# Performance work log

Measured on AMD Instinct MI355X. Metric: run time of the kernel, lower is better.

## Reference

```python
import jax, jax.numpy as jnp
import numpy as np

N_NODES = 20000      # rows of mask
MAX_DEG = 64         # padded slots per node (softmax dim)
DEG = 16             # actual edges per node
E = N_NODES * DEG    # 320000 edges
D_X = 64
D_REF = 64
IN_SIZE = D_X + D_REF   # 128
OUT_SIZE = 64
NEG_FILL = -9e15


def setup_inputs() -> dict:
    key = jax.random.key(0)
    k1, k2, k3, k4 = jax.random.split(key, 4)
    x = jax.random.normal(k1, (E, D_X), dtype=jnp.float32)
    ref = jax.random.normal(k2, (E, D_REF), dtype=jnp.float32)
    mask = jnp.ones((N_NODES, MAX_DEG), dtype=bool)  # only its shape is used
    # valid (node, slot) pairs: each node owns slots 0..DEG-1
    rows = jnp.repeat(jnp.arange(N_NODES, dtype=jnp.int32), DEG)
    cols = jnp.tile(jnp.arange(DEG, dtype=jnp.int32), N_NODES)
    x_idx = jnp.stack([rows, cols], axis=0)  # [2, E]
    # Linear(in_size, out_size) params (torch convention: W [out, in])
    bound = 1.0 / np.sqrt(IN_SIZE)
    W = jax.random.uniform(k3, (OUT_SIZE, IN_SIZE), jnp.float32, -bound, bound)
    b = jax.random.uniform(k4, (OUT_SIZE,), jnp.float32, -bound, bound)
    return {"x": x, "ref": ref, "mask": mask, "x_idx": x_idx, "W": W, "b": b}


def reference(x, ref, mask, x_idx, W, b):
    # w = tanh(Linear(cat([x, ref], -1)))  -> [E, OUT]
    w = jnp.tanh(jnp.concatenate([x, ref], axis=-1) @ W.T + b)
    # scatter into dense [N, MAX_DEG, OUT] padded with a huge negative value
    dense = jnp.full(mask.shape + (w.shape[-1],), NEG_FILL, dtype=w.dtype)
    dense = dense.at[x_idx[0], x_idx[1]].set(w)
    # softmax over the slot dimension (dim=-2), then gather back to edges
    dense = jax.nn.softmax(dense, axis=-2)
    return dense[x_idx[0], x_idx[1]]
```

## Files before the change

kernel.cpp:

```cpp
#include <hip/hip_runtime.h>


#define DEG 16
#define DCH 64
#define KDIM 128
#define NPW 10

typedef __bf16 bf16x8 __attribute__((ext_vector_type(8)));
typedef float f32x4 __attribute__((ext_vector_type(4)));

__device__ __forceinline__ bf16x8 cvt8(f32x4 a, f32x4 b) {
    bf16x8 r;
    r[0] = (__bf16)a[0]; r[1] = (__bf16)a[1]; r[2] = (__bf16)a[2]; r[3] = (__bf16)a[3];
    r[4] = (__bf16)b[0]; r[5] = (__bf16)b[1]; r[6] = (__bf16)b[2]; r[7] = (__bf16)b[3];
    return r;
}

__device__ __forceinline__ void load_node(const float* __restrict__ xr,
                                          const float* __restrict__ rr,
                                          f32x4* __restrict__ raw) {
    raw[0] = *(const f32x4*)(xr);
    raw[1] = *(const f32x4*)(xr + 4);
    raw[2] = *(const f32x4*)(xr + 32);
    raw[3] = *(const f32x4*)(xr + 36);
    raw[4] = *(const f32x4*)(rr);
    raw[5] = *(const f32x4*)(rr + 4);
    raw[6] = *(const f32x4*)(rr + 32);
    raw[7] = *(const f32x4*)(rr + 36);
}

__global__ __launch_bounds__(256, 2) void attn_fused(
    const float* __restrict__ x, const float* __restrict__ ref,
    const float* __restrict__ W, const float* __restrict__ bias,
    float* __restrict__ out)
{
    const int lane = threadIdx.x & 63;
    const int wid  = blockIdx.x * 4 + (threadIdx.x >> 6);
    const int r16  = lane & 15;
    const int g    = lane >> 4;

    bf16x8 Bf[4][4];
#pragma unroll
    for (int u = 0; u < 4; ++u) {
        const float* wr = W + (u * 16 + r16) * KDIM;
#pragma unroll
        for (int t = 0; t < 4; ++t) {
            const float* p = wr + t * 32 + g * 8;
            Bf[t][u] = cvt8(*(const f32x4*)p, *(const f32x4*)(p + 4));
        }
    }
    float bv[4];
#pragma unroll
    for (int u = 0; u < 4; ++u) bv[u] = bias[u * 16 + r16];

    const size_t e0 = (size_t)wid * (NPW * DEG);

    f32x4 bufA[8], bufB[8];
    load_node(x + (e0 + r16) * DCH + g * 8, ref + (e0 + r16) * DCH + g * 8, bufA);

#pragma unroll
    for (int ni = 0; ni < NPW; ++ni) {
        f32x4* cur = (ni & 1) ? bufB : bufA;
        f32x4* nxt = (ni & 1) ? bufA : bufB;
        if (ni + 1 < NPW) {
            const size_t e = e0 + (size_t)(ni + 1) * DEG;
            load_node(x + (e + r16) * DCH + g * 8, ref + (e + r16) * DCH + g * 8, nxt);
        }

        f32x4 acc[4];
#pragma unroll
        for (int u = 0; u < 4; ++u)
            acc[u] = (f32x4){bv[u], bv[u], bv[u], bv[u]};
#pragma unroll
        for (int t = 0; t < 4; ++t) {
            bf16x8 Af = cvt8(cur[2 * t], cur[2 * t + 1]);
#pragma unroll
            for (int u = 0; u < 4; ++u)
                acc[u] = __builtin_amdgcn_mfma_f32_16x16x32_bf16(Af, Bf[t][u], acc[u], 0, 0, 0);
        }

        float* ob = out + (e0 + (size_t)ni * DEG) * DCH;
#pragma unroll
        for (int u = 0; u < 4; ++u) {
            float p[4];
            float s = 0.f;
#pragma unroll
            for (int r = 0; r < 4; ++r) {
                float z = acc[u][r];
                float e = __expf(2.f * z);
                float w = 1.f - 2.f * __builtin_amdgcn_rcpf(e + 1.f);
                p[r] = __expf(w);
                s += p[r];
            }
            s += __shfl_xor(s, 16);
            s += __shfl_xor(s, 32);
            float inv = __builtin_amdgcn_rcpf(s);
#pragma unroll
            for (int r = 0; r < 4; ++r)
                ob[(g * 4 + r) * DCH + u * 16 + r16] = p[r] * inv;
        }
    }
}

extern "C" void kernel_launch(void* const* d_in, const int* in_sizes, int n_in,
                              void* d_out, int out_size, void* d_ws, size_t ws_size,
                              hipStream_t stream) {
    const float* x   = (const float*)d_in[0];
    const float* ref = (const float*)d_in[1];
    const float* W   = (const float*)d_in[4];
    const float* b   = (const float*)d_in[5];
    float* out = (float*)d_out;

    attn_fused<<<500, 256, 0, stream>>>(x, ref, W, b, out);
}
```

Measured before the change: 223.0 us.

## Stage node inputs via async global-to-LDS loads with swizzled double buffering

Replaces per-lane register prefetch of x/ref rows with global_load_lds direct-to-LDS copies into two per-wave XOR-swizzled slots. Waits are driven by explicit vmcnt counters, and each node's tile is read back from LDS before issuing the copy for node k+2. The goal is fully coalesced 16-byte loads and deeper prefetch without using registers. The cost is 64KB of LDS per block, which may limit occupancy, plus fragile hand-tuned waitcnt values and an extra LDS round trip.

```diff
diff --git a/kernel.cpp b/kernel.cpp
--- a/kernel.cpp
+++ b/kernel.cpp
@@ -1,10 +1,11 @@
 #include <hip/hip_runtime.h>
+#include <stdint.h>
 
 
 #define DEG 16
 #define DCH 64
 #define KDIM 128
-#define NPW 10
+#define ITERS 10
 
 typedef __bf16 bf16x8 __attribute__((ext_vector_type(8)));
 typedef float f32x4 __attribute__((ext_vector_type(4)));
@@ -16,17 +17,25 @@
     return r;
 }
 
-__device__ __forceinline__ void load_node(const float* __restrict__ xr,
-                                          const float* __restrict__ rr,
-                                          f32x4* __restrict__ raw) {
-    raw[0] = *(const f32x4*)(xr);
-    raw[1] = *(const f32x4*)(xr + 4);
-    raw[2] = *(const f32x4*)(xr + 32);
-    raw[3] = *(const f32x4*)(xr + 36);
-    raw[4] = *(const f32x4*)(rr);
-    raw[5] = *(const f32x4*)(rr + 4);
-    raw[6] = *(const f32x4*)(rr + 32);
-    raw[7] = *(const f32x4*)(rr + 36);
+__device__ __forceinline__ void gload16(const float* gsrc, void* ldst) {
+    __builtin_amdgcn_global_load_lds(
+        (const __attribute__((address_space(1))) uint32_t*)gsrc,
+        (__attribute__((address_space(3))) uint32_t*)ldst, 16, 0, 0);
+}
+
+__device__ __forceinline__ void stage_node(const float* __restrict__ x,
+                                           const float* __restrict__ ref,
+                                           int node, char* slot, int lane) {
+    const int rq = lane >> 4;
+    const int cb = (lane & 15) * 16;
+#pragma unroll
+    for (int i = 0; i < 8; ++i) {
+        const int r  = (i & 3) * 4 + rq;
+        const int sc = cb ^ ((r & 7) << 5);
+        const float* base = (i < 4) ? x : ref;
+        const float* src  = base + (size_t)(node * DEG + r) * DCH + (sc >> 2);
+        gload16(src, slot + i * 1024);
+    }
 }
 
 __global__ __launch_bounds__(256, 2) void attn_fused(
@@ -34,10 +43,14 @@
     const float* __restrict__ W, const float* __restrict__ bias,
     float* __restrict__ out)
 {
+    __shared__ __align__(16) char smem[65536];
+
     const int lane = threadIdx.x & 63;
-    const int wid  = blockIdx.x * 4 + (threadIdx.x >> 6);
+    const int wv   = threadIdx.x >> 6;
+    const int wid  = blockIdx.x * 4 + wv;
     const int r16  = lane & 15;
     const int g    = lane >> 4;
+    const int sw16 = (r16 & 7) << 5;
 
     bf16x8 Bf[4][4];
 #pragma unroll
@@ -53,33 +66,47 @@
 #pragma unroll
     for (int u = 0; u < 4; ++u) bv[u] = bias[u * 16 + r16];
 
-    const size_t e0 = (size_t)wid * (NPW * DEG);
+    char* slot0 = smem + wv * 16384;
+    char* slot1 = slot0 + 8192;
+    const int base = wid * ITERS;
 
-    f32x4 bufA[8], bufB[8];
-    load_node(x + (e0 + r16) * DCH + g * 8, ref + (e0 + r16) * DCH + g * 8, bufA);
+    stage_node(x, ref, base + 0, slot0, lane);
+    stage_node(x, ref, base + 1, slot1, lane);
+    __builtin_amdgcn_sched_barrier(0);
 
+#pragma unroll 1
+    for (int k = 0; k < ITERS; ++k) {
+        if (k == 0) { asm volatile("s_waitcnt vmcnt(8)" ::: "memory"); }
+        else        { asm volatile("s_waitcnt vmcnt(24)" ::: "memory"); }
+        __builtin_amdgcn_sched_barrier(0);
+
+        char* S = (k & 1) ? slot1 : slot0;
+
+        bf16x8 Af[4];
 #pragma unroll
-    for (int ni = 0; ni < NPW; ++ni) {
-        f32x4* cur = (ni & 1) ? bufB : bufA;
-        f32x4* nxt = (ni & 1) ? bufA : bufB;
-        if (ni + 1 < NPW) {
-            const size_t e = e0 + (size_t)(ni + 1) * DEG;
-            load_node(x + (e + r16) * DCH + g * 8, ref + (e + r16) * DCH + g * 8, nxt);
+        for (int t = 0; t < 4; ++t) {
+            const int colb = (t & 1) * 128 + g * 32;
+            const char* p = S + (t >> 1) * 4096 + r16 * 256 + (colb ^ sw16);
+            f32x4 a0 = *(const f32x4*)p;
+            f32x4 a1 = *(const f32x4*)(p + 16);
+            Af[t] = cvt8(a0, a1);
         }
+        asm volatile("s_waitcnt lgkmcnt(0)" ::: "memory");
+        __builtin_amdgcn_sched_barrier(0);
+        if (k + 2 < ITERS) stage_node(x, ref, base + k + 2, S, lane);
+        __builtin_amdgcn_sched_barrier(0);
 
         f32x4 acc[4];
 #pragma unroll
         for (int u = 0; u < 4; ++u)
             acc[u] = (f32x4){bv[u], bv[u], bv[u], bv[u]};
 #pragma unroll
-        for (int t = 0; t < 4; ++t) {
-            bf16x8 Af = cvt8(cur[2 * t], cur[2 * t + 1]);
+        for (int t = 0; t < 4; ++t)
 #pragma unroll
             for (int u = 0; u < 4; ++u)
-                acc[u] = __builtin_amdgcn_mfma_f32_16x16x32_bf16(Af, Bf[t][u], acc[u], 0, 0, 0);
-        }
+                acc[u] = __builtin_amdgcn_mfma_f32_16x16x32_bf16(Af[t], Bf[t][u], acc[u], 0, 0, 0);
 
-        float* ob = out + (e0 + (size_t)ni * DEG) * DCH;
+        float* ob = out + (size_t)(base + k) * DEG * DCH;
 #pragma unroll
         for (int u = 0; u < 4; ++u) {
             float p[4];
```

Result: no change. 224.1 us (+0.5%).
